# Optimization experiments

Measured on AMD Instinct MI355X. Metric: run time of the kernel, lower is better.

The kernel has to match this reference:

```python
import jax, jax.numpy as jnp
import numpy as np

GRID_SIZE = 10
DEGREE = 3


def bspline_basis(x, grid_size=GRID_SIZE, degree=DEGREE):
    """Cox-de Boor B-spline basis on a uniform grid over [-1, 1].
    x: (...,) -> (..., grid_size + degree)
    """
    h = 2.0 / grid_size
    # extended knot vector, length grid_size + 2*degree + 1
    knots = jnp.arange(-degree, grid_size + degree + 1, dtype=x.dtype) * h - 1.0
    # keep inputs inside the grid support (standard KAN practice)
    x = jnp.clip(x, -1.0, 1.0 - 1e-6)
    xe = x[..., None]
    b = ((xe >= knots[:-1]) & (xe < knots[1:])).astype(x.dtype)  # degree-0, (..., K-1)
    for d in range(1, degree + 1):
        left = (xe - knots[: -(d + 1)]) / (knots[d:-1] - knots[: -(d + 1)]) * b[..., :-1]
        right = (knots[d + 1:] - xe) / (knots[d + 1:] - knots[1:-d]) * b[..., 1:]
        b = left + right
    return b  # (..., grid_size + degree)


def setup_inputs() -> dict:
    key = jax.random.key(0)
    k1, k2, k3 = jax.random.split(key, 3)
    B, S, IN, OUT, E = 4, 2048, 256, 256, 8
    n_basis = GRID_SIZE + DEGREE
    x = jax.random.normal(k1, (B, S, IN), dtype=jnp.float32)
    coeff = jax.random.normal(k2, (E, n_basis), dtype=jnp.float32) * 0.1
    gating_weights = jax.random.normal(k3, (IN, OUT, E), dtype=jnp.float32)
    return {"x": x, "coeff": coeff, "gating_weights": gating_weights}


def reference(x, coeff, gating_weights):
    # spline experts: elementwise basis eval, then per-expert linear combo
    basis = bspline_basis(x)                              # (B, S, I, n_basis)
    expert_outputs = jnp.einsum('bsin,en->bsie', basis, coeff)  # (B, S, I, E)
    gates = jax.nn.softmax(gating_weights, axis=-1)       # (I, O, E)
    out = jnp.einsum('bsie,ioe->bso', expert_outputs, gates)
    return out
```

## Files before the change

kernel.cpp:

```cpp
#include <hip/hip_runtime.h>

typedef __attribute__((ext_vector_type(8))) short short8;
typedef __attribute__((ext_vector_type(4))) float f32x4;

#define IN_DIM 256
#define OUT_DIM 256
#define NB 16
#define KDIM (IN_DIM * NB)
#define TM 32
#define TN 128
#define BK 128
#define STEPS (IN_DIM / 8)
#define ABUF (TM * BK * 2)
#define BBUF (TN * BK * 2)

__device__ __forceinline__ unsigned short f2bf(float f) {
  union { float f; unsigned int u; } v; v.f = f;
  unsigned int r = v.u + 0x7fffu + ((v.u >> 16) & 1u);
  return (unsigned short)(r >> 16);
}

__device__ __forceinline__ void glds16(const void* g, void* l) {
  __builtin_amdgcn_global_load_lds((__attribute__((address_space(1))) const void*)g,
                                   (__attribute__((address_space(3))) void*)l, 16, 0, 0);
}

__device__ __forceinline__ void spline_row(float xv, unsigned* d) {
  float xc = fminf(fmaxf(xv, -1.0f), 1.0f - 1e-6f);
  float u = (xc + 1.0f) * 5.0f;
  int c = (int)u;
  c = c > 9 ? 9 : (c < 0 ? 0 : c);
  float tt = u - (float)c;
  float omt = 1.0f - tt;
  float t2 = tt * tt, t3 = t2 * tt;
  float b0 = omt * omt * omt * (1.0f / 6.0f);
  float b1 = (3.0f * t3 - 6.0f * t2 + 4.0f) * (1.0f / 6.0f);
  float b2 = (-3.0f * t3 + 3.0f * t2 + 3.0f * tt + 1.0f) * (1.0f / 6.0f);
  float b3 = t3 * (1.0f / 6.0f);
  unsigned h0 = f2bf(b0), h1 = f2bf(b1), h2 = f2bf(b2), h3 = f2bf(b3);
  const int a = c >> 1;
  const bool odd = (c & 1) != 0;
  unsigned p01 = h0 | (h1 << 16);
  unsigned p23 = h2 | (h3 << 16);
  unsigned A0 = odd ? (h0 << 16) : p01;
  unsigned A1 = odd ? (h1 | (h2 << 16)) : p23;
  unsigned A2 = odd ? h3 : 0u;
#pragma unroll
  for (int j = 0; j < 8; ++j) {
    unsigned v = (j == a) ? A0 : 0u;
    v = (j == a + 1) ? A1 : v;
    v = (j == a + 2) ? A2 : v;
    d[j] = v;
  }
}

__global__ __launch_bounds__(256) void kan_prep(const float* __restrict__ coeff,
                                                const float* __restrict__ gw,
                                                unsigned short* __restrict__ BmT) {
  __shared__ float csh[104];
  __shared__ unsigned short tile[16][256];
  const int t = threadIdx.x;
  if (t < 104) csh[t] = coeff[t];
  __syncthreads();
  const int otile = blockIdx.x, itile = blockIdx.y;
  const int il = t >> 4, ol = t & 15;
  const int i = itile * 16 + il;
  const int o = otile * 16 + ol;
  const float* g = gw + (size_t)(i * OUT_DIM + o) * 8;
  float4 g0 = *(const float4*)g;
  float4 g1 = *(const float4*)(g + 4);
  float ge[8] = {g0.x, g0.y, g0.z, g0.w, g1.x, g1.y, g1.z, g1.w};
  float mx = ge[0];
#pragma unroll
  for (int e = 1; e < 8; ++e) mx = fmaxf(mx, ge[e]);
  float p[8]; float s = 0.f;
#pragma unroll
  for (int e = 0; e < 8; ++e) { p[e] = __expf(ge[e] - mx); s += p[e]; }
  const float inv = 1.0f / s;
  unsigned short row[16];
#pragma unroll
  for (int n = 0; n < 13; ++n) {
    float w = 0.f;
#pragma unroll
    for (int e = 0; e < 8; ++e) w += p[e] * csh[e * 13 + n];
    row[n] = f2bf(w * inv);
  }
  row[13] = 0; row[14] = 0; row[15] = 0;
  int4* dst = (int4*)&tile[ol][il * 16];
  dst[0] = *(const int4*)&row[0];
  dst[1] = *(const int4*)&row[8];
  __syncthreads();
  const int oo = t >> 4, ck = t & 15;
  int4 v0 = *(const int4*)&tile[oo][ck * 16];
  int4 v1 = *(const int4*)&tile[oo][ck * 16 + 8];
  int4* out4 = (int4*)(BmT + (size_t)(otile * 16 + oo) * KDIM + itile * 256 + ck * 16);
  out4[0] = v0;
  out4[1] = v1;
}

__global__ __launch_bounds__(256, 2) void kan_gemm(const float* __restrict__ x,
                                                   const unsigned short* __restrict__ BmT,
                                                   float* __restrict__ out) {
  __shared__ unsigned short Ash[2][TM * BK];
  __shared__ unsigned short Bsh[2][TN * BK];

  const int t = threadIdx.x;
  const int lane = t & 63;
  const int wave = t >> 6;
  const int wn = wave;
  const int mb = blockIdx.x * TM;
  const int ob = blockIdx.y * TN;

  const int r = t & 31;
  const int il = t >> 5;
  const float* xptr = x + (size_t)(mb + r) * IN_DIM + il;
  char* const abase = (char*)&Ash[0][0] + r * 256;
  const int msw = r & 7;
  const int aw0 = ((2 * il + 0) ^ msw) << 4;
  const int aw1 = ((2 * il + 1) ^ msw) << 4;

  const unsigned short* bgbase =
      BmT + (size_t)(ob + (t >> 4)) * KDIM + ((t & 15) ^ ((t >> 4) & 7)) * 8;
  char* const bl = (char*)&Bsh[0][0] + wave * 1024;

  f32x4 acc[2][2];
#pragma unroll
  for (int a = 0; a < 2; ++a)
#pragma unroll
    for (int b = 0; b < 2; ++b) acc[a][b] = (f32x4){0.f, 0.f, 0.f, 0.f};

  int aoff[2], boff[2];
#pragma unroll
  for (int f = 0; f < 2; ++f) {
    const int ro = f * 16 + (lane & 15);
    aoff[f] = ro * 256 + (((lane >> 4) ^ (ro & 7)) << 4);
    const int bo = wn * 32 + f * 16 + (lane & 15);
    boff[f] = bo * 256 + (((lane >> 4) ^ (bo & 7)) << 4);
  }

  {
#pragma unroll
    for (int q = 0; q < 8; ++q)
      glds16(bgbase + (size_t)q * 16 * KDIM, bl + q * 4096);
    float xv = *xptr;
    unsigned d[8];
    spline_row(xv, d);
    *(int4*)(abase + aw0) = *(const int4*)&d[0];
    *(int4*)(abase + aw1) = *(const int4*)&d[4];
    asm volatile("s_waitcnt vmcnt(0)" ::: "memory");
  }

  for (int s = 0; s < STEPS; ++s) {
    __syncthreads();
    const int cur = s & 1;
    float xn = 0.f;
    if (s + 1 < STEPS) {
      xn = xptr[(s + 1) * 8];
#pragma unroll
      for (int q = 0; q < 8; ++q)
        glds16(bgbase + (size_t)(s + 1) * BK + (size_t)q * 16 * KDIM,
               bl + (1 - cur) * BBUF + q * 4096);
    }
    const char* Ac = (const char*)&Ash[0][0] + cur * ABUF;
    const char* Bc = (const char*)&Bsh[0][0] + cur * BBUF;
    __builtin_amdgcn_s_setprio(1);
#pragma unroll
    for (int kc = 0; kc < 4; ++kc) {
      short8 af[2], bfr[2];
#pragma unroll
      for (int f = 0; f < 2; ++f) af[f] = *(const short8*)(Ac + (aoff[f] ^ (kc << 6)));
#pragma unroll
      for (int f = 0; f < 2; ++f) bfr[f] = *(const short8*)(Bc + (boff[f] ^ (kc << 6)));
#pragma unroll
      for (int mf = 0; mf < 2; ++mf)
#pragma unroll
        for (int nf = 0; nf < 2; ++nf)
          acc[mf][nf] = __builtin_amdgcn_mfma_f32_16x16x32_bf16(af[mf], bfr[nf], acc[mf][nf], 0, 0, 0);
    }
    __builtin_amdgcn_s_setprio(0);
    if (s + 1 < STEPS) {
      unsigned d[8];
      spline_row(xn, d);
      char* an = abase + (1 - cur) * ABUF;
      *(int4*)(an + aw0) = *(const int4*)&d[0];
      *(int4*)(an + aw1) = *(const int4*)&d[4];
    }
  }

#pragma unroll
  for (int mf = 0; mf < 2; ++mf)
#pragma unroll
    for (int nf = 0; nf < 2; ++nf)
#pragma unroll
      for (int q = 0; q < 4; ++q) {
        int row = mb + mf * 16 + ((lane >> 4) << 2) + q;
        int col = ob + wn * 32 + nf * 16 + (lane & 15);
        out[(size_t)row * OUT_DIM + col] = acc[mf][nf][q];
      }
}

extern "C" void kernel_launch(void* const* d_in, const int* in_sizes, int n_in,
                              void* d_out, int out_size, void* d_ws, size_t ws_size,
                              hipStream_t stream) {
  const float* x     = (const float*)d_in[0];
  const float* coeff = (const float*)d_in[1];
  const float* gw    = (const float*)d_in[2];
  float* out = (float*)d_out;
  unsigned short* BmT = (unsigned short*)d_ws;

  kan_prep<<<dim3(16, 16), dim3(256), 0, stream>>>(coeff, gw, BmT);
  dim3 grid(8192 / TM, OUT_DIM / TN);
  kan_gemm<<<grid, dim3(256), 0, stream>>>(x, BmT, out);
}
```

Measured before the change: 105.1 us.

## Reshape GEMM tile to 128x64 with 8 waves in a 4x2 layout

```diff
diff --git a/kernel.cpp b/kernel.cpp
--- a/kernel.cpp
+++ b/kernel.cpp
@@ -7,8 +7,8 @@
 #define OUT_DIM 256
 #define NB 16
 #define KDIM (IN_DIM * NB)
-#define TM 32
-#define TN 128
+#define TM 128
+#define TN 64
 #define BK 128
 #define STEPS (IN_DIM / 8)
 #define ABUF (TM * BK * 2)
@@ -98,7 +98,7 @@
   out4[1] = v1;
 }
 
-__global__ __launch_bounds__(256, 2) void kan_gemm(const float* __restrict__ x,
+__global__ __launch_bounds__(512, 1) void kan_gemm(const float* __restrict__ x,
                                                    const unsigned short* __restrict__ BmT,
                                                    float* __restrict__ out) {
   __shared__ unsigned short Ash[2][TM * BK];
@@ -107,17 +107,14 @@
   const int t = threadIdx.x;
   const int lane = t & 63;
   const int wave = t >> 6;
-  const int wn = wave;
+  const int wm = wave >> 1, wn = wave & 1;
   const int mb = blockIdx.x * TM;
   const int ob = blockIdx.y * TN;
 
-  const int r = t & 31;
-  const int il = t >> 5;
-  const float* xptr = x + (size_t)(mb + r) * IN_DIM + il;
-  char* const abase = (char*)&Ash[0][0] + r * 256;
+  const int r = t & 127;
+  const int il = t >> 7;
+  const float* xptr = x + (size_t)(mb + r) * IN_DIM + 2 * il;
   const int msw = r & 7;
-  const int aw0 = ((2 * il + 0) ^ msw) << 4;
-  const int aw1 = ((2 * il + 1) ^ msw) << 4;
 
   const unsigned short* bgbase =
       BmT + (size_t)(ob + (t >> 4)) * KDIM + ((t & 15) ^ ((t >> 4) & 7)) * 8;
@@ -132,34 +129,35 @@
   int aoff[2], boff[2];
 #pragma unroll
   for (int f = 0; f < 2; ++f) {
-    const int ro = f * 16 + (lane & 15);
+    const int ro = wm * 32 + f * 16 + (lane & 15);
     aoff[f] = ro * 256 + (((lane >> 4) ^ (ro & 7)) << 4);
     const int bo = wn * 32 + f * 16 + (lane & 15);
     boff[f] = bo * 256 + (((lane >> 4) ^ (bo & 7)) << 4);
   }
 
   {
-#pragma unroll
-    for (int q = 0; q < 8; ++q)
-      glds16(bgbase + (size_t)q * 16 * KDIM, bl + q * 4096);
-    float xv = *xptr;
-    unsigned d[8];
-    spline_row(xv, d);
-    *(int4*)(abase + aw0) = *(const int4*)&d[0];
-    *(int4*)(abase + aw1) = *(const int4*)&d[4];
+    glds16(bgbase, bl);
+    glds16(bgbase + (size_t)32 * KDIM, bl + 8192);
+    float2 xv = *(const float2*)xptr;
+    unsigned d0[8], d1[8];
+    spline_row(xv.x, d0);
+    spline_row(xv.y, d1);
+    char* an = (char*)&Ash[0][0] + r * 256;
+    *(int4*)(an + (((4 * il + 0) ^ msw) << 4)) = *(const int4*)&d0[0];
+    *(int4*)(an + (((4 * il + 1) ^ msw) << 4)) = *(const int4*)&d0[4];
+    *(int4*)(an + (((4 * il + 2) ^ msw) << 4)) = *(const int4*)&d1[0];
+    *(int4*)(an + (((4 * il + 3) ^ msw) << 4)) = *(const int4*)&d1[4];
     asm volatile("s_waitcnt vmcnt(0)" ::: "memory");
   }
 
   for (int s = 0; s < STEPS; ++s) {
     __syncthreads();
     const int cur = s & 1;
-    float xn = 0.f;
+    float2 xn;
     if (s + 1 < STEPS) {
-      xn = xptr[(s + 1) * 8];
-#pragma unroll
-      for (int q = 0; q < 8; ++q)
-        glds16(bgbase + (size_t)(s + 1) * BK + (size_t)q * 16 * KDIM,
-               bl + (1 - cur) * BBUF + q * 4096);
+      xn = *(const float2*)(xptr + (s + 1) * 8);
+      glds16(bgbase + (size_t)(s + 1) * BK, bl + (1 - cur) * BBUF);
+      glds16(bgbase + (size_t)(s + 1) * BK + (size_t)32 * KDIM, bl + (1 - cur) * BBUF + 8192);
     }
     const char* Ac = (const char*)&Ash[0][0] + cur * ABUF;
     const char* Bc = (const char*)&Bsh[0][0] + cur * BBUF;
@@ -179,11 +177,14 @@
     }
     __builtin_amdgcn_s_setprio(0);
     if (s + 1 < STEPS) {
-      unsigned d[8];
-      spline_row(xn, d);
-      char* an = abase + (1 - cur) * ABUF;
-      *(int4*)(an + aw0) = *(const int4*)&d[0];
-      *(int4*)(an + aw1) = *(const int4*)&d[4];
+      unsigned d0[8], d1[8];
+      spline_row(xn.x, d0);
+      spline_row(xn.y, d1);
+      char* an = (char*)&Ash[0][0] + (1 - cur) * ABUF + r * 256;
+      *(int4*)(an + (((4 * il + 0) ^ msw) << 4)) = *(const int4*)&d0[0];
+      *(int4*)(an + (((4 * il + 1) ^ msw) << 4)) = *(const int4*)&d0[4];
+      *(int4*)(an + (((4 * il + 2) ^ msw) << 4)) = *(const int4*)&d1[0];
+      *(int4*)(an + (((4 * il + 3) ^ msw) << 4)) = *(const int4*)&d1[4];
     }
   }
 
@@ -193,7 +194,7 @@
     for (int nf = 0; nf < 2; ++nf)
 #pragma unroll
       for (int q = 0; q < 4; ++q) {
-        int row = mb + mf * 16 + ((lane >> 4) << 2) + q;
+        int row = mb + wm * 32 + mf * 16 + ((lane >> 4) << 2) + q;
         int col = ob + wn * 32 + nf * 16 + (lane & 15);
         out[(size_t)row * OUT_DIM + col] = acc[mf][nf][q];
       }
@@ -210,5 +211,5 @@
 
   kan_prep<<<dim3(16, 16), dim3(256), 0, stream>>>(coeff, gw, BmT);
   dim3 grid(8192 / TM, OUT_DIM / TN);
-  kan_gemm<<<grid, dim3(256), 0, stream>>>(x, BmT, out);
-}
+  kan_gemm<<<grid, dim3(512), 0, stream>>>(x, BmT, out);
+}
```

New measurement: 114.1 us. +8.6%, slower.

## Split K across two blocks with atomic accumulation and halve BK tile

Applied to the files above, without the earlier changes.

```diff
diff --git a/kernel.cpp b/kernel.cpp
--- a/kernel.cpp
+++ b/kernel.cpp
@@ -9,8 +9,10 @@
 #define KDIM (IN_DIM * NB)
 #define TM 32
 #define TN 128
-#define BK 128
-#define STEPS (IN_DIM / 8)
+#define BK 64
+#define KSPLIT 2
+#define IPER (IN_DIM / KSPLIT)
+#define STEPS (IPER / 4)
 #define ABUF (TM * BK * 2)
 #define BBUF (TN * BK * 2)
 
@@ -56,10 +58,18 @@
 
 __global__ __launch_bounds__(256) void kan_prep(const float* __restrict__ coeff,
                                                 const float* __restrict__ gw,
-                                                unsigned short* __restrict__ BmT) {
+                                                unsigned short* __restrict__ BmT,
+                                                float* __restrict__ out) {
   __shared__ float csh[104];
   __shared__ unsigned short tile[16][256];
   const int t = threadIdx.x;
+  {
+    const int bid = blockIdx.y * 16 + blockIdx.x;
+    float4 z; z.x = z.y = z.z = z.w = 0.f;
+    float4* ob = (float4*)out;
+#pragma unroll
+    for (int j = 0; j < 8; ++j) ob[(size_t)bid * 2048 + j * 256 + t] = z;
+  }
   if (t < 104) csh[t] = coeff[t];
   __syncthreads();
   const int otile = blockIdx.x, itile = blockIdx.y;
@@ -98,7 +108,7 @@
   out4[1] = v1;
 }
 
-__global__ __launch_bounds__(256, 2) void kan_gemm(const float* __restrict__ x,
+__global__ __launch_bounds__(256, 4) void kan_gemm(const float* __restrict__ x,
                                                    const unsigned short* __restrict__ BmT,
                                                    float* __restrict__ out) {
   __shared__ unsigned short Ash[2][TM * BK];
@@ -110,17 +120,19 @@
   const int wn = wave;
   const int mb = blockIdx.x * TM;
   const int ob = blockIdx.y * TN;
+  const int i0 = blockIdx.z * IPER;
 
   const int r = t & 31;
-  const int il = t >> 5;
-  const float* xptr = x + (size_t)(mb + r) * IN_DIM + il;
-  char* const abase = (char*)&Ash[0][0] + r * 256;
+  const int il = (t >> 5) & 3;
+  const bool astage = t < 128;
+  const float* xptr = x + (size_t)(mb + r) * IN_DIM + i0 + il;
+  char* const abase = (char*)&Ash[0][0] + r * 128;
   const int msw = r & 7;
   const int aw0 = ((2 * il + 0) ^ msw) << 4;
   const int aw1 = ((2 * il + 1) ^ msw) << 4;
 
   const unsigned short* bgbase =
-      BmT + (size_t)(ob + (t >> 4)) * KDIM + ((t & 15) ^ ((t >> 4) & 7)) * 8;
+      BmT + (size_t)(ob + (t >> 3)) * KDIM + i0 * NB + ((t & 7) ^ ((t >> 3) & 7)) * 8;
   char* const bl = (char*)&Bsh[0][0] + wave * 1024;
 
   f32x4 acc[2][2];
@@ -133,20 +145,22 @@
 #pragma unroll
   for (int f = 0; f < 2; ++f) {
     const int ro = f * 16 + (lane & 15);
-    aoff[f] = ro * 256 + (((lane >> 4) ^ (ro & 7)) << 4);
+    aoff[f] = ro * 128 + (((lane >> 4) ^ (ro & 7)) << 4);
     const int bo = wn * 32 + f * 16 + (lane & 15);
-    boff[f] = bo * 256 + (((lane >> 4) ^ (bo & 7)) << 4);
+    boff[f] = bo * 128 + (((lane >> 4) ^ (bo & 7)) << 4);
   }
 
   {
 #pragma unroll
-    for (int q = 0; q < 8; ++q)
-      glds16(bgbase + (size_t)q * 16 * KDIM, bl + q * 4096);
-    float xv = *xptr;
-    unsigned d[8];
-    spline_row(xv, d);
-    *(int4*)(abase + aw0) = *(const int4*)&d[0];
-    *(int4*)(abase + aw1) = *(const int4*)&d[4];
+    for (int q = 0; q < 4; ++q)
+      glds16(bgbase + (size_t)q * 32 * KDIM, bl + q * 4096);
+    if (astage) {
+      float xv = *xptr;
+      unsigned d[8];
+      spline_row(xv, d);
+      *(int4*)(abase + aw0) = *(const int4*)&d[0];
+      *(int4*)(abase + aw1) = *(const int4*)&d[4];
+    }
     asm volatile("s_waitcnt vmcnt(0)" ::: "memory");
   }
 
@@ -155,17 +169,17 @@
     const int cur = s & 1;
     float xn = 0.f;
     if (s + 1 < STEPS) {
-      xn = xptr[(s + 1) * 8];
-#pragma unroll
-      for (int q = 0; q < 8; ++q)
-        glds16(bgbase + (size_t)(s + 1) * BK + (size_t)q * 16 * KDIM,
+      if (astage) xn = xptr[(s + 1) * 4];
+#pragma unroll
+      for (int q = 0; q < 4; ++q)
+        glds16(bgbase + (size_t)(s + 1) * BK + (size_t)q * 32 * KDIM,
                bl + (1 - cur) * BBUF + q * 4096);
     }
     const char* Ac = (const char*)&Ash[0][0] + cur * ABUF;
     const char* Bc = (const char*)&Bsh[0][0] + cur * BBUF;
     __builtin_amdgcn_s_setprio(1);
 #pragma unroll
-    for (int kc = 0; kc < 4; ++kc) {
+    for (int kc = 0; kc < 2; ++kc) {
       short8 af[2], bfr[2];
 #pragma unroll
       for (int f = 0; f < 2; ++f) af[f] = *(const short8*)(Ac + (aoff[f] ^ (kc << 6)));
@@ -178,7 +192,7 @@
           acc[mf][nf] = __builtin_amdgcn_mfma_f32_16x16x32_bf16(af[mf], bfr[nf], acc[mf][nf], 0, 0, 0);
     }
     __builtin_amdgcn_s_setprio(0);
-    if (s + 1 < STEPS) {
+    if (astage && s + 1 < STEPS) {
       unsigned d[8];
       spline_row(xn, d);
       char* an = abase + (1 - cur) * ABUF;
@@ -195,7 +209,7 @@
       for (int q = 0; q < 4; ++q) {
         int row = mb + mf * 16 + ((lane >> 4) << 2) + q;
         int col = ob + wn * 32 + nf * 16 + (lane & 15);
-        out[(size_t)row * OUT_DIM + col] = acc[mf][nf][q];
+        atomicAdd(out + (size_t)row * OUT_DIM + col, acc[mf][nf][q]);
       }
 }
 
@@ -208,7 +222,7 @@
   float* out = (float*)d_out;
   unsigned short* BmT = (unsigned short*)d_ws;
 
-  kan_prep<<<dim3(16, 16), dim3(256), 0, stream>>>(coeff, gw, BmT);
-  dim3 grid(8192 / TM, OUT_DIM / TN);
+  kan_prep<<<dim3(16, 16), dim3(256), 0, stream>>>(coeff, gw, BmT, out);
+  dim3 grid(8192 / TM, OUT_DIM / TN, KSPLIT);
   kan_gemm<<<grid, dim3(256), 0, stream>>>(x, BmT, out);
 }
```

New measurement: 110.2 us. 1.05x slower.

## Fold coefficients into per-interval cubic polynomials, shrink GEMM K to experts

Applied to the files above, without the earlier changes.

```diff
diff --git a/kernel.cpp b/kernel.cpp
--- a/kernel.cpp
+++ b/kernel.cpp
@@ -5,14 +5,10 @@
 
 #define IN_DIM 256
 #define OUT_DIM 256
-#define NB 16
-#define KDIM (IN_DIM * NB)
+#define K2 2048
 #define TM 32
 #define TN 128
-#define BK 128
-#define STEPS (IN_DIM / 8)
-#define ABUF (TM * BK * 2)
-#define BBUF (TN * BK * 2)
+#define NSLICE 64
 
 __device__ __forceinline__ unsigned short f2bf(float f) {
   union { float f; unsigned int u; } v; v.f = f;
@@ -20,52 +16,12 @@
   return (unsigned short)(r >> 16);
 }
 
-__device__ __forceinline__ void glds16(const void* g, void* l) {
-  __builtin_amdgcn_global_load_lds((__attribute__((address_space(1))) const void*)g,
-                                   (__attribute__((address_space(3))) void*)l, 16, 0, 0);
-}
-
-__device__ __forceinline__ void spline_row(float xv, unsigned* d) {
-  float xc = fminf(fmaxf(xv, -1.0f), 1.0f - 1e-6f);
-  float u = (xc + 1.0f) * 5.0f;
-  int c = (int)u;
-  c = c > 9 ? 9 : (c < 0 ? 0 : c);
-  float tt = u - (float)c;
-  float omt = 1.0f - tt;
-  float t2 = tt * tt, t3 = t2 * tt;
-  float b0 = omt * omt * omt * (1.0f / 6.0f);
-  float b1 = (3.0f * t3 - 6.0f * t2 + 4.0f) * (1.0f / 6.0f);
-  float b2 = (-3.0f * t3 + 3.0f * t2 + 3.0f * tt + 1.0f) * (1.0f / 6.0f);
-  float b3 = t3 * (1.0f / 6.0f);
-  unsigned h0 = f2bf(b0), h1 = f2bf(b1), h2 = f2bf(b2), h3 = f2bf(b3);
-  const int a = c >> 1;
-  const bool odd = (c & 1) != 0;
-  unsigned p01 = h0 | (h1 << 16);
-  unsigned p23 = h2 | (h3 << 16);
-  unsigned A0 = odd ? (h0 << 16) : p01;
-  unsigned A1 = odd ? (h1 | (h2 << 16)) : p23;
-  unsigned A2 = odd ? h3 : 0u;
-#pragma unroll
-  for (int j = 0; j < 8; ++j) {
-    unsigned v = (j == a) ? A0 : 0u;
-    v = (j == a + 1) ? A1 : v;
-    v = (j == a + 2) ? A2 : v;
-    d[j] = v;
-  }
-}
-
-__global__ __launch_bounds__(256) void kan_prep(const float* __restrict__ coeff,
-                                                const float* __restrict__ gw,
-                                                unsigned short* __restrict__ BmT) {
-  __shared__ float csh[104];
-  __shared__ unsigned short tile[16][256];
+__global__ __launch_bounds__(256) void kan_prep(const float* __restrict__ gw,
+                                                unsigned short* __restrict__ G2) {
   const int t = threadIdx.x;
-  if (t < 104) csh[t] = coeff[t];
-  __syncthreads();
-  const int otile = blockIdx.x, itile = blockIdx.y;
-  const int il = t >> 4, ol = t & 15;
-  const int i = itile * 16 + il;
-  const int o = otile * 16 + ol;
+  const int il = t & 15, ol = t >> 4;
+  const int i = blockIdx.y * 16 + il;
+  const int o = blockIdx.x * 16 + ol;
   const float* g = gw + (size_t)(i * OUT_DIM + o) * 8;
   float4 g0 = *(const float4*)g;
   float4 g1 = *(const float4*)(g + 4);
@@ -77,51 +33,66 @@
 #pragma unroll
   for (int e = 0; e < 8; ++e) { p[e] = __expf(ge[e] - mx); s += p[e]; }
   const float inv = 1.0f / s;
-  unsigned short row[16];
+  unsigned w[4];
 #pragma unroll
-  for (int n = 0; n < 13; ++n) {
-    float w = 0.f;
+  for (int q = 0; q < 4; ++q)
+    w[q] = (unsigned)f2bf(p[2 * q] * inv) | ((unsigned)f2bf(p[2 * q + 1] * inv) << 16);
+  *(int4*)(G2 + (size_t)o * K2 + i * 8) = *(const int4*)w;
+}
+
+__device__ __forceinline__ short8 evalA(float xv, const float* __restrict__ PT) {
+  float xc = fminf(fmaxf(xv, -1.0f), 1.0f - 1e-6f);
+  float u = (xc + 1.0f) * 5.0f;
+  int c = (int)u;
+  c = c > 9 ? 9 : c;
+  float tt = u - (float)c;
+  const float* p = PT + c * 36;
+  float pv[8];
 #pragma unroll
-    for (int e = 0; e < 8; ++e) w += p[e] * csh[e * 13 + n];
-    row[n] = f2bf(w * inv);
+  for (int e = 0; e < 8; ++e) {
+    f32x4 a = *(const f32x4*)(p + e * 4);
+    pv[e] = fmaf(fmaf(fmaf(a[3], tt, a[2]), tt, a[1]), tt, a[0]);
   }
-  row[13] = 0; row[14] = 0; row[15] = 0;
-  int4* dst = (int4*)&tile[ol][il * 16];
-  dst[0] = *(const int4*)&row[0];
-  dst[1] = *(const int4*)&row[8];
-  __syncthreads();
-  const int oo = t >> 4, ck = t & 15;
-  int4 v0 = *(const int4*)&tile[oo][ck * 16];
-  int4 v1 = *(const int4*)&tile[oo][ck * 16 + 8];
-  int4* out4 = (int4*)(BmT + (size_t)(otile * 16 + oo) * KDIM + itile * 256 + ck * 16);
-  out4[0] = v0;
-  out4[1] = v1;
+  union { unsigned w[4]; short8 s; } r;
+#pragma unroll
+  for (int q = 0; q < 4; ++q) {
+    unsigned lo = (__float_as_uint(pv[2 * q]) + 0x8000u) >> 16;
+    unsigned hi = (__float_as_uint(pv[2 * q + 1]) + 0x8000u) & 0xFFFF0000u;
+    r.w[q] = lo | hi;
+  }
+  return r.s;
 }
 
 __global__ __launch_bounds__(256, 2) void kan_gemm(const float* __restrict__ x,
-                                                   const unsigned short* __restrict__ BmT,
+                                                   const float* __restrict__ coeff,
+                                                   const unsigned short* __restrict__ G2,
                                                    float* __restrict__ out) {
-  __shared__ unsigned short Ash[2][TM * BK];
-  __shared__ unsigned short Bsh[2][TN * BK];
+  __shared__ __align__(16) float PT[360];
 
   const int t = threadIdx.x;
+  if (t < 80) {
+    const int c = t >> 3, e = t & 7;
+    const float C0 = coeff[e * 13 + c],     C1 = coeff[e * 13 + c + 1];
+    const float C2 = coeff[e * 13 + c + 2], C3 = coeff[e * 13 + c + 3];
+    float* p = &PT[c * 36 + e * 4];
+    p[0] = (C0 + 4.0f * C1 + C2) * (1.0f / 6.0f);
+    p[1] = (C2 - C0) * 0.5f;
+    p[2] = (C0 - 2.0f * C1 + C2) * 0.5f;
+    p[3] = (C3 - C0 + 3.0f * (C1 - C2)) * (1.0f / 6.0f);
+  }
+  __syncthreads();
+
   const int lane = t & 63;
-  const int wave = t >> 6;
-  const int wn = wave;
+  const int wn = t >> 6;
   const int mb = blockIdx.x * TM;
   const int ob = blockIdx.y * TN;
+  const int rl = lane & 15;
+  const int iq = lane >> 4;
 
-  const int r = t & 31;
-  const int il = t >> 5;
-  const float* xptr = x + (size_t)(mb + r) * IN_DIM + il;
-  char* const abase = (char*)&Ash[0][0] + r * 256;
-  const int msw = r & 7;
-  const int aw0 = ((2 * il + 0) ^ msw) << 4;
-  const int aw1 = ((2 * il + 1) ^ msw) << 4;
-
-  const unsigned short* bgbase =
-      BmT + (size_t)(ob + (t >> 4)) * KDIM + ((t & 15) ^ ((t >> 4) & 7)) * 8;
-  char* const bl = (char*)&Bsh[0][0] + wave * 1024;
+  const float* xp0 = x + (size_t)(mb + rl) * IN_DIM + iq;
+  const float* xp1 = xp0 + 16 * IN_DIM;
+  const unsigned short* bp0 = G2 + (size_t)(ob + wn * 32 + rl) * K2 + iq * 8;
+  const unsigned short* bp1 = bp0 + 16 * K2;
 
   f32x4 acc[2][2];
 #pragma unroll
@@ -129,62 +100,18 @@
 #pragma unroll
     for (int b = 0; b < 2; ++b) acc[a][b] = (f32x4){0.f, 0.f, 0.f, 0.f};
 
-  int aoff[2], boff[2];
-#pragma unroll
-  for (int f = 0; f < 2; ++f) {
-    const int ro = f * 16 + (lane & 15);
-    aoff[f] = ro * 256 + (((lane >> 4) ^ (ro & 7)) << 4);
-    const int bo = wn * 32 + f * 16 + (lane & 15);
-    boff[f] = bo * 256 + (((lane >> 4) ^ (bo & 7)) << 4);
-  }
-
-  {
-#pragma unroll
-    for (int q = 0; q < 8; ++q)
-      glds16(bgbase + (size_t)q * 16 * KDIM, bl + q * 4096);
-    float xv = *xptr;
-    unsigned d[8];
-    spline_row(xv, d);
-    *(int4*)(abase + aw0) = *(const int4*)&d[0];
-    *(int4*)(abase + aw1) = *(const int4*)&d[4];
-    asm volatile("s_waitcnt vmcnt(0)" ::: "memory");
-  }
-
-  for (int s = 0; s < STEPS; ++s) {
-    __syncthreads();
-    const int cur = s & 1;
-    float xn = 0.f;
-    if (s + 1 < STEPS) {
-      xn = xptr[(s + 1) * 8];
-#pragma unroll
-      for (int q = 0; q < 8; ++q)
-        glds16(bgbase + (size_t)(s + 1) * BK + (size_t)q * 16 * KDIM,
-               bl + (1 - cur) * BBUF + q * 4096);
-    }
-    const char* Ac = (const char*)&Ash[0][0] + cur * ABUF;
-    const char* Bc = (const char*)&Bsh[0][0] + cur * BBUF;
-    __builtin_amdgcn_s_setprio(1);
-#pragma unroll
-    for (int kc = 0; kc < 4; ++kc) {
-      short8 af[2], bfr[2];
-#pragma unroll
-      for (int f = 0; f < 2; ++f) af[f] = *(const short8*)(Ac + (aoff[f] ^ (kc << 6)));
-#pragma unroll
-      for (int f = 0; f < 2; ++f) bfr[f] = *(const short8*)(Bc + (boff[f] ^ (kc << 6)));
-#pragma unroll
-      for (int mf = 0; mf < 2; ++mf)
-#pragma unroll
-        for (int nf = 0; nf < 2; ++nf)
-          acc[mf][nf] = __builtin_amdgcn_mfma_f32_16x16x32_bf16(af[mf], bfr[nf], acc[mf][nf], 0, 0, 0);
-    }
-    __builtin_amdgcn_s_setprio(0);
-    if (s + 1 < STEPS) {
-      unsigned d[8];
-      spline_row(xn, d);
-      char* an = abase + (1 - cur) * ABUF;
-      *(int4*)(an + aw0) = *(const int4*)&d[0];
-      *(int4*)(an + aw1) = *(const int4*)&d[4];
-    }
+#pragma unroll 2
+  for (int s = 0; s < NSLICE; ++s) {
+    const float x0 = xp0[s * 4];
+    const float x1 = xp1[s * 4];
+    const short8 b0 = *(const short8*)(bp0 + s * 32);
+    const short8 b1 = *(const short8*)(bp1 + s * 32);
+    const short8 a0 = evalA(x0, PT);
+    const short8 a1 = evalA(x1, PT);
+    acc[0][0] = __builtin_amdgcn_mfma_f32_16x16x32_bf16(a0, b0, acc[0][0], 0, 0, 0);
+    acc[0][1] = __builtin_amdgcn_mfma_f32_16x16x32_bf16(a0, b1, acc[0][1], 0, 0, 0);
+    acc[1][0] = __builtin_amdgcn_mfma_f32_16x16x32_bf16(a1, b0, acc[1][0], 0, 0, 0);
+    acc[1][1] = __builtin_amdgcn_mfma_f32_16x16x32_bf16(a1, b1, acc[1][1], 0, 0, 0);
   }
 
 #pragma unroll
@@ -193,8 +120,8 @@
     for (int nf = 0; nf < 2; ++nf)
 #pragma unroll
       for (int q = 0; q < 4; ++q) {
-        int row = mb + mf * 16 + ((lane >> 4) << 2) + q;
-        int col = ob + wn * 32 + nf * 16 + (lane & 15);
+        int row = mb + mf * 16 + (iq << 2) + q;
+        int col = ob + wn * 32 + nf * 16 + rl;
         out[(size_t)row * OUT_DIM + col] = acc[mf][nf][q];
       }
 }
@@ -206,9 +133,9 @@
   const float* coeff = (const float*)d_in[1];
   const float* gw    = (const float*)d_in[2];
   float* out = (float*)d_out;
-  unsigned short* BmT = (unsigned short*)d_ws;
+  unsigned short* G2 = (unsigned short*)d_ws;
 
-  kan_prep<<<dim3(16, 16), dim3(256), 0, stream>>>(coeff, gw, BmT);
+  kan_prep<<<dim3(16, 16), dim3(256), 0, stream>>>(gw, G2);
   dim3 grid(8192 / TM, OUT_DIM / TN);
-  kan_gemm<<<grid, dim3(256), 0, stream>>>(x, BmT, out);
+  kan_gemm<<<grid, dim3(256), 0, stream>>>(x, coeff, G2, out);
 }
```

New measurement: 122.3 us. 16.4% more time.
